# Performance work log

Hardware: AMD Instinct MI355X
Metric: run time of the kernel (lower is better)

## Reference

```python
import jax, jax.numpy as jnp
import numpy as np

N_STREAMS = 8
SINKHORN_ITER = 20
KERNEL_SIZE = 5
BANDWIDTH = 0.5
PAD = KERNEL_SIZE // 2
EPS = 1e-8


def _gaussian_kernel():
    x = jnp.arange(KERNEL_SIZE, dtype=jnp.float32) - KERNEL_SIZE // 2
    xx, yy = jnp.meshgrid(x, x, indexing='ij')
    k = jnp.exp(-(xx ** 2 + yy ** 2) / (2.0 * BANDWIDTH ** 2))
    k = k / k.sum()
    return k.reshape(1, 1, KERNEL_SIZE, KERNEL_SIZE)  # OIHW


def setup_inputs() -> dict:
    key = jax.random.key(0)
    B, H, W = 32, 128, 128
    log_H_res = jax.random.normal(key, (B, N_STREAMS * N_STREAMS, H, W), dtype=jnp.float32)
    return {"log_H_res": log_H_res, "gaussian_kernel": _gaussian_kernel()}


def reference(log_H_res, gaussian_kernel):
    B, C, H, W = log_H_res.shape
    n = N_STREAMS
    H_lin = jnp.exp(log_H_res.reshape(B, n, n, H, W))

    def smooth(m):
        # m: (B, n, H, W) linear-domain marginal; circular pad + 5x5 Gaussian conv
        x = m.reshape(B * n, 1, H, W)
        x = jnp.pad(x, ((0, 0), (0, 0), (PAD, PAD), (PAD, PAD)), mode='wrap')
        y = jax.lax.conv_general_dilated(
            x, gaussian_kernel, window_strides=(1, 1), padding='VALID',
            dimension_numbers=('NCHW', 'OIHW', 'NCHW'))
        return y.reshape(B, n, H, W)

    def body(_, Hl):
        row = smooth(Hl.sum(axis=2))[:, :, None]   # (B, n, 1, H, W)
        Hl = Hl / (row + EPS)
        col = smooth(Hl.sum(axis=1))[:, None]      # (B, 1, n, H, W)
        Hl = Hl / (col + EPS)
        return Hl

    H_lin = jax.lax.fori_loop(0, SINKHORN_ITER, body, H_lin)
    # faithful to original: log then exp with eps stabilization
    H_star = jnp.exp(jnp.log(H_lin + EPS))
    return H_star  # (B, n, n, H, W)
```

## Files before the change

### kernel.cpp

```cpp
#include <hip/hip_runtime.h>

#define NS    8
#define HGT   128
#define WID   128
#define HW    (HGT * WID)
#define BATCH 32
#define EPSV  1e-8f
#define ITERS 20

#define TH   8
#define LH   (TH + 4)
#define LW   132

typedef float4 f4;
typedef _Float16 half4 __attribute__((ext_vector_type(4)));

__global__ __launch_bounds__(256) void k_init(const float* __restrict__ logH,
                                              _Float16* __restrict__ H0h,
                                              float* __restrict__ u,
                                              float* __restrict__ v,
                                              float* __restrict__ mrow) {
    int gid = blockIdx.x * 256 + threadIdx.x;
    int e = gid * 4;
    int p = e & (HW - 1);
    int c = (e >> 14) & 7;
    int b = e >> 17;
    int base = ((b * NS + c) * NS) * HW + p;
    f4 s = {0.f, 0.f, 0.f, 0.f};
#pragma unroll
    for (int j = 0; j < NS; ++j) {
        f4 l = *(const f4*)(logH + base + j * HW);
        f4 ev;
        ev.x = __expf(l.x); ev.y = __expf(l.y);
        ev.z = __expf(l.z); ev.w = __expf(l.w);
        half4 h;
        h.x = (_Float16)ev.x; h.y = (_Float16)ev.y;
        h.z = (_Float16)ev.z; h.w = (_Float16)ev.w;
        *(half4*)(H0h + base + j * HW) = h;
        s.x += ev.x; s.y += ev.y; s.z += ev.z; s.w += ev.w;
    }
    f4 one = {1.f, 1.f, 1.f, 1.f};
    *(f4*)(u + e) = one;
    *(f4*)(v + e) = one;
    *(f4*)(mrow + e) = s;
}

__device__ __forceinline__ void stage_and_smooth(
        const float* __restrict__ m_in, const float* __restrict__ gk,
        float* __restrict__ a, int b, int ty0, int tid,
        float tile[NS][LH][LW], float wk[25], f4 av[NS], bool write_a) {
    if (tid < 25) wk[tid] = gk[tid];

#pragma unroll
    for (int c = 0; c < NS; ++c) {
        const float* src = m_in + (b * NS + c) * HW;
        for (int t = tid; t < LH * 32; t += 256) {
            int ly = t >> 5, lxq = t & 31;
            int gh = (ty0 + ly - 2 + HGT) & (HGT - 1);
            f4 val = *(const f4*)(src + gh * WID + lxq * 4);
            float* dst = &tile[c][ly][2 + lxq * 4];
            dst[0] = val.x; dst[1] = val.y; dst[2] = val.z; dst[3] = val.w;
        }
        if (tid < LH * 4) {
            int ly = tid >> 2, e = tid & 3;
            int gh = (ty0 + ly - 2 + HGT) & (HGT - 1);
            int x  = (e < 2) ? (126 + e) : (e - 2);
            int hx = (e < 2) ? e : (128 + e);
            tile[c][ly][hx] = src[gh * WID + x];
        }
    }
    __syncthreads();

    int lxq = tid & 31;
    int ly  = tid >> 5;
    int p   = (ty0 + ly) * WID + lxq * 4;

#pragma unroll
    for (int c = 0; c < NS; ++c) {
        float s0 = 0.f, s1 = 0.f, s2 = 0.f, s3 = 0.f;
#pragma unroll
        for (int dy = 0; dy < 5; ++dy) {
            const float* row = &tile[c][ly + dy][lxq * 4];
            f4 A = *(const f4*)row;
            f4 B = *(const f4*)(row + 4);
            float vv[8] = {A.x, A.y, A.z, A.w, B.x, B.y, B.z, B.w};
#pragma unroll
            for (int dx = 0; dx < 5; ++dx) {
                float w = wk[dy * 5 + dx];
                s0 += w * vv[dx];
                s1 += w * vv[dx + 1];
                s2 += w * vv[dx + 2];
                s3 += w * vv[dx + 3];
            }
        }
        int ai = (b * NS + c) * HW + p;
        f4 ao = *(const f4*)(a + ai);
        f4 un;
        un.x = ao.x / (s0 + EPSV);
        un.y = ao.y / (s1 + EPSV);
        un.z = ao.z / (s2 + EPSV);
        un.w = ao.w / (s3 + EPSV);
        if (write_a) *(f4*)(a + ai) = un;
        av[c] = un;
    }
}

template <int ROWSTEP>
__global__ __launch_bounds__(256) void k_step(const float* __restrict__ m_in,
                                              float* __restrict__ a,
                                              const float* __restrict__ bvec,
                                              float* __restrict__ m_out,
                                              const _Float16* __restrict__ H0h,
                                              const float* __restrict__ gk) {
    __shared__ float tile[NS][LH][LW];
    __shared__ float wk[25];
    int tid = threadIdx.x;
    int b   = blockIdx.z;
    int ty0 = blockIdx.y * TH;

    f4 av[NS];
    stage_and_smooth(m_in, gk, a, b, ty0, tid, tile, wk, av, true);

    int lxq = tid & 31;
    int ly  = tid >> 5;
    int p   = (ty0 + ly) * WID + lxq * 4;

    f4 acc[NS];
#pragma unroll
    for (int cp = 0; cp < NS; ++cp) acc[cp] = f4{0.f, 0.f, 0.f, 0.f};
    const _Float16* Hb = H0h + b * NS * NS * HW + p;
#pragma unroll
    for (int c = 0; c < NS; ++c) {
        f4 x = av[c];
#pragma unroll
        for (int cp = 0; cp < NS; ++cp) {
            int ch = ROWSTEP ? (c * NS + cp) : (cp * NS + c);
            half4 h = *(const half4*)(Hb + ch * HW);
            acc[cp].x += (float)h.x * x.x;
            acc[cp].y += (float)h.y * x.y;
            acc[cp].z += (float)h.z * x.z;
            acc[cp].w += (float)h.w * x.w;
        }
    }
#pragma unroll
    for (int cp = 0; cp < NS; ++cp) {
        int oi = (b * NS + cp) * HW + p;
        f4 bv = *(const f4*)(bvec + oi);
        f4 o;
        o.x = bv.x * acc[cp].x;
        o.y = bv.y * acc[cp].y;
        o.z = bv.z * acc[cp].z;
        o.w = bv.w * acc[cp].w;
        *(f4*)(m_out + oi) = o;
    }
}

__global__ __launch_bounds__(256) void k_last(const float* __restrict__ m_in,
                                              float* __restrict__ v,
                                              const float* __restrict__ u,
                                              const float* __restrict__ logH,
                                              float* __restrict__ out,
                                              const float* __restrict__ gk) {
    __shared__ float tile[NS][LH][LW];
    __shared__ float wk[25];
    int tid = threadIdx.x;
    int b   = blockIdx.z;
    int ty0 = blockIdx.y * TH;

    f4 av[NS];
    stage_and_smooth(m_in, gk, v, b, ty0, tid, tile, wk, av, false);

    int lxq = tid & 31;
    int ly  = tid >> 5;
    int p   = (ty0 + ly) * WID + lxq * 4;

    const float* Lb = logH + b * NS * NS * HW + p;
    float* Ob = out + b * NS * NS * HW + p;
#pragma unroll
    for (int i = 0; i < NS; ++i) {
        f4 uu = *(const f4*)(u + (b * NS + i) * HW + p);
#pragma unroll
        for (int j = 0; j < NS; ++j) {
            f4 l = *(const f4*)(Lb + (i * NS + j) * HW);
            f4 o;
            o.x = expf(l.x) * uu.x * av[j].x + EPSV;
            o.y = expf(l.y) * uu.y * av[j].y + EPSV;
            o.z = expf(l.z) * uu.z * av[j].z + EPSV;
            o.w = expf(l.w) * uu.w * av[j].w + EPSV;
            *(f4*)(Ob + (i * NS + j) * HW) = o;
        }
    }
}

extern "C" void kernel_launch(void* const* d_in, const int* in_sizes, int n_in,
                              void* d_out, int out_size, void* d_ws, size_t ws_size,
                              hipStream_t stream) {
    const float* logH = (const float*)d_in[0];
    const float* gk   = (const float*)d_in[1];
    float* out = (float*)d_out;
    _Float16* H0h = (_Float16*)d_out;
    float* ws = (float*)d_ws;
    const int VEC = BATCH * NS * HW;
    float* u    = ws;
    float* v    = ws + VEC;
    float* mrow = ws + 2 * VEC;
    float* mcol = ws + 3 * VEC;

    k_init<<<VEC / 4 / 256, 256, 0, stream>>>(logH, H0h, u, v, mrow);

    dim3 grid(1, HGT / TH, BATCH);
    for (int it = 0; it < ITERS; ++it) {
        k_step<1><<<grid, 256, 0, stream>>>(mrow, u, v, mcol, H0h, gk);
        if (it != ITERS - 1) {
            k_step<0><<<grid, 256, 0, stream>>>(mcol, v, u, mrow, H0h, gk);
        } else {
            k_last<<<grid, 256, 0, stream>>>(mcol, v, u, logH, out, gk);
        }
    }
}
```

Before: 1.465 ms.

## Fuse all Sinkhorn iterations into one persistent cooperative kernel with grid sync

Replaces the 41 separate kernel launches with a single cooperative kernel that keeps the u and v scaling vectors in registers across iterations. Stages are separated by grid-wide syncs, which removes launch overhead and the global-memory round trips for u and v. The grid is 16x32 = 512 blocks with 256 threads and about 50KB of shared memory each, so it relies on every block being co-resident. If the cooperative launch fails, the code falls back to the multi-kernel path.

```diff
diff --git a/kernel.cpp b/kernel.cpp
--- a/kernel.cpp
+++ b/kernel.cpp
@@ -1,4 +1,7 @@
 #include <hip/hip_runtime.h>
+#include <hip/hip_cooperative_groups.h>
+
+namespace cg = cooperative_groups;
 
 #define NS    8
 #define HGT   128
@@ -14,6 +17,186 @@
 
 typedef float4 f4;
 typedef _Float16 half4 __attribute__((ext_vector_type(4)));
+
+__device__ __forceinline__ void stage_tile(const float* __restrict__ m_in,
+                                           int b, int ty0, int tid,
+                                           float tile[NS][LH][LW]) {
+#pragma unroll
+    for (int c = 0; c < NS; ++c) {
+        const float* src = m_in + (b * NS + c) * HW;
+        for (int t = tid; t < LH * 32; t += 256) {
+            int ly = t >> 5, lxq = t & 31;
+            int gh = (ty0 + ly - 2 + HGT) & (HGT - 1);
+            f4 val = *(const f4*)(src + gh * WID + lxq * 4);
+            float* dst = &tile[c][ly][2 + lxq * 4];
+            dst[0] = val.x; dst[1] = val.y; dst[2] = val.z; dst[3] = val.w;
+        }
+        if (tid < LH * 4) {
+            int ly = tid >> 2, e = tid & 3;
+            int gh = (ty0 + ly - 2 + HGT) & (HGT - 1);
+            int x  = (e < 2) ? (126 + e) : (e - 2);
+            int hx = (e < 2) ? e : (128 + e);
+            tile[c][ly][hx] = src[gh * WID + x];
+        }
+    }
+}
+
+__device__ __forceinline__ f4 conv5(const float (*tc)[LW], const float* wk,
+                                    int ly, int lxq) {
+    float s0 = 0.f, s1 = 0.f, s2 = 0.f, s3 = 0.f;
+#pragma unroll
+    for (int dy = 0; dy < 5; ++dy) {
+        const float* row = &tc[ly + dy][lxq * 4];
+        f4 A = *(const f4*)row;
+        f4 B = *(const f4*)(row + 4);
+        float vv[8] = {A.x, A.y, A.z, A.w, B.x, B.y, B.z, B.w};
+#pragma unroll
+        for (int dx = 0; dx < 5; ++dx) {
+            float w = wk[dy * 5 + dx];
+            s0 += w * vv[dx];
+            s1 += w * vv[dx + 1];
+            s2 += w * vv[dx + 2];
+            s3 += w * vv[dx + 3];
+        }
+    }
+    return f4{s0, s1, s2, s3};
+}
+
+__global__ __launch_bounds__(256, 2) void k_sink_all(
+        const float* __restrict__ logH, _Float16* __restrict__ H0h,
+        float* __restrict__ mrow, float* __restrict__ mcol,
+        const float* __restrict__ gk, float* __restrict__ out) {
+    cg::grid_group grid = cg::this_grid();
+    __shared__ float tile[NS][LH][LW];
+    __shared__ float wk[25];
+    int tid = threadIdx.x;
+    int ty0 = blockIdx.x * TH;
+    int b   = blockIdx.y;
+    if (tid < 25) wk[tid] = gk[tid];
+
+    int lxq = tid & 31;
+    int ly  = tid >> 5;
+    int p   = (ty0 + ly) * WID + lxq * 4;
+
+    const float* Lb = logH + (b * NS * NS) * HW + p;
+    _Float16*    Hb = H0h  + (b * NS * NS) * HW + p;
+
+    f4 u[NS], v[NS];
+
+#pragma unroll
+    for (int i = 0; i < NS; ++i) {
+        f4 si = {0.f, 0.f, 0.f, 0.f};
+#pragma unroll
+        for (int j = 0; j < NS; ++j) {
+            f4 l = *(const f4*)(Lb + (i * NS + j) * HW);
+            f4 ev;
+            ev.x = __expf(l.x); ev.y = __expf(l.y);
+            ev.z = __expf(l.z); ev.w = __expf(l.w);
+            half4 h;
+            h.x = (_Float16)ev.x; h.y = (_Float16)ev.y;
+            h.z = (_Float16)ev.z; h.w = (_Float16)ev.w;
+            *(half4*)(Hb + (i * NS + j) * HW) = h;
+            si.x += ev.x; si.y += ev.y; si.z += ev.z; si.w += ev.w;
+        }
+        *(f4*)(mrow + (b * NS + i) * HW + p) = si;
+        u[i] = f4{1.f, 1.f, 1.f, 1.f};
+        v[i] = f4{1.f, 1.f, 1.f, 1.f};
+    }
+    grid.sync();
+
+    for (int it = 0; it < ITERS; ++it) {
+        stage_tile(mrow, b, ty0, tid, tile);
+        __syncthreads();
+#pragma unroll
+        for (int c = 0; c < NS; ++c) {
+            f4 s = conv5(tile[c], wk, ly, lxq);
+            u[c].x /= (s.x + EPSV);
+            u[c].y /= (s.y + EPSV);
+            u[c].z /= (s.z + EPSV);
+            u[c].w /= (s.w + EPSV);
+        }
+        {
+            f4 acc[NS];
+#pragma unroll
+            for (int cp = 0; cp < NS; ++cp) acc[cp] = f4{0.f, 0.f, 0.f, 0.f};
+#pragma unroll
+            for (int c = 0; c < NS; ++c) {
+                f4 x = u[c];
+#pragma unroll
+                for (int cp = 0; cp < NS; ++cp) {
+                    half4 h = *(const half4*)(Hb + (c * NS + cp) * HW);
+                    acc[cp].x += (float)h.x * x.x;
+                    acc[cp].y += (float)h.y * x.y;
+                    acc[cp].z += (float)h.z * x.z;
+                    acc[cp].w += (float)h.w * x.w;
+                }
+            }
+#pragma unroll
+            for (int cp = 0; cp < NS; ++cp) {
+                f4 o;
+                o.x = v[cp].x * acc[cp].x;
+                o.y = v[cp].y * acc[cp].y;
+                o.z = v[cp].z * acc[cp].z;
+                o.w = v[cp].w * acc[cp].w;
+                *(f4*)(mcol + (b * NS + cp) * HW + p) = o;
+            }
+        }
+        grid.sync();
+
+        stage_tile(mcol, b, ty0, tid, tile);
+        __syncthreads();
+#pragma unroll
+        for (int c = 0; c < NS; ++c) {
+            f4 s = conv5(tile[c], wk, ly, lxq);
+            v[c].x /= (s.x + EPSV);
+            v[c].y /= (s.y + EPSV);
+            v[c].z /= (s.z + EPSV);
+            v[c].w /= (s.w + EPSV);
+        }
+        if (it != ITERS - 1) {
+            f4 acc[NS];
+#pragma unroll
+            for (int cp = 0; cp < NS; ++cp) acc[cp] = f4{0.f, 0.f, 0.f, 0.f};
+#pragma unroll
+            for (int c = 0; c < NS; ++c) {
+                f4 x = v[c];
+#pragma unroll
+                for (int cp = 0; cp < NS; ++cp) {
+                    half4 h = *(const half4*)(Hb + (cp * NS + c) * HW);
+                    acc[cp].x += (float)h.x * x.x;
+                    acc[cp].y += (float)h.y * x.y;
+                    acc[cp].z += (float)h.z * x.z;
+                    acc[cp].w += (float)h.w * x.w;
+                }
+            }
+#pragma unroll
+            for (int cp = 0; cp < NS; ++cp) {
+                f4 o;
+                o.x = u[cp].x * acc[cp].x;
+                o.y = u[cp].y * acc[cp].y;
+                o.z = u[cp].z * acc[cp].z;
+                o.w = u[cp].w * acc[cp].w;
+                *(f4*)(mrow + (b * NS + cp) * HW + p) = o;
+            }
+            grid.sync();
+        }
+    }
+
+    float* Ob = out + (b * NS * NS) * HW + p;
+#pragma unroll
+    for (int i = 0; i < NS; ++i) {
+#pragma unroll
+        for (int j = 0; j < NS; ++j) {
+            f4 l = *(const f4*)(Lb + (i * NS + j) * HW);
+            f4 o;
+            o.x = expf(l.x) * u[i].x * v[j].x + EPSV;
+            o.y = expf(l.y) * u[i].y * v[j].y + EPSV;
+            o.z = expf(l.z) * u[i].z * v[j].z + EPSV;
+            o.w = expf(l.w) * u[i].w * v[j].w + EPSV;
+            *(f4*)(Ob + (i * NS + j) * HW) = o;
+        }
+    }
+}
 
 __global__ __launch_bounds__(256) void k_init(const float* __restrict__ logH,
                                               _Float16* __restrict__ H0h,
@@ -50,25 +233,7 @@
         float* __restrict__ a, int b, int ty0, int tid,
         float tile[NS][LH][LW], float wk[25], f4 av[NS], bool write_a) {
     if (tid < 25) wk[tid] = gk[tid];
-
-#pragma unroll
-    for (int c = 0; c < NS; ++c) {
-        const float* src = m_in + (b * NS + c) * HW;
-        for (int t = tid; t < LH * 32; t += 256) {
-            int ly = t >> 5, lxq = t & 31;
-            int gh = (ty0 + ly - 2 + HGT) & (HGT - 1);
-            f4 val = *(const f4*)(src + gh * WID + lxq * 4);
-            float* dst = &tile[c][ly][2 + lxq * 4];
-            dst[0] = val.x; dst[1] = val.y; dst[2] = val.z; dst[3] = val.w;
-        }
-        if (tid < LH * 4) {
-            int ly = tid >> 2, e = tid & 3;
-            int gh = (ty0 + ly - 2 + HGT) & (HGT - 1);
-            int x  = (e < 2) ? (126 + e) : (e - 2);
-            int hx = (e < 2) ? e : (128 + e);
-            tile[c][ly][hx] = src[gh * WID + x];
-        }
-    }
+    stage_tile(m_in, b, ty0, tid, tile);
     __syncthreads();
 
     int lxq = tid & 31;
@@ -77,29 +242,14 @@
 
 #pragma unroll
     for (int c = 0; c < NS; ++c) {
-        float s0 = 0.f, s1 = 0.f, s2 = 0.f, s3 = 0.f;
-#pragma unroll
-        for (int dy = 0; dy < 5; ++dy) {
-            const float* row = &tile[c][ly + dy][lxq * 4];
-            f4 A = *(const f4*)row;
-            f4 B = *(const f4*)(row + 4);
-            float vv[8] = {A.x, A.y, A.z, A.w, B.x, B.y, B.z, B.w};
-#pragma unroll
-            for (int dx = 0; dx < 5; ++dx) {
-                float w = wk[dy * 5 + dx];
-                s0 += w * vv[dx];
-                s1 += w * vv[dx + 1];
-                s2 += w * vv[dx + 2];
-                s3 += w * vv[dx + 3];
-            }
-        }
+        f4 s = conv5(tile[c], wk, ly, lxq);
         int ai = (b * NS + c) * HW + p;
         f4 ao = *(const f4*)(a + ai);
         f4 un;
-        un.x = ao.x / (s0 + EPSV);
-        un.y = ao.y / (s1 + EPSV);
-        un.z = ao.z / (s2 + EPSV);
-        un.w = ao.w / (s3 + EPSV);
+        un.x = ao.x / (s.x + EPSV);
+        un.y = ao.y / (s.y + EPSV);
+        un.z = ao.z / (s.z + EPSV);
+        un.w = ao.w / (s.w + EPSV);
         if (write_a) *(f4*)(a + ai) = un;
         av[c] = un;
     }
@@ -201,20 +351,31 @@
     _Float16* H0h = (_Float16*)d_out;
     float* ws = (float*)d_ws;
     const int VEC = BATCH * NS * HW;
-    float* u    = ws;
-    float* v    = ws + VEC;
-    float* mrow = ws + 2 * VEC;
-    float* mcol = ws + 3 * VEC;
-
-    k_init<<<VEC / 4 / 256, 256, 0, stream>>>(logH, H0h, u, v, mrow);
+
+    float* mrow = ws;
+    float* mcol = ws + VEC;
+    void* args[] = {(void*)&logH, (void*)&H0h, (void*)&mrow, (void*)&mcol,
+                    (void*)&gk, (void*)&out};
+    hipError_t err = hipLaunchCooperativeKernel(k_sink_all,
+                                                dim3(HGT / TH, BATCH, 1),
+                                                dim3(256, 1, 1),
+                                                args, 0, stream);
+    if (err == hipSuccess) return;
+
+    float* u     = ws;
+    float* v     = ws + VEC;
+    float* mrow2 = ws + 2 * (size_t)VEC;
+    float* mcol2 = ws + 3 * (size_t)VEC;
+
+    k_init<<<VEC / 4 / 256, 256, 0, stream>>>(logH, H0h, u, v, mrow2);
 
     dim3 grid(1, HGT / TH, BATCH);
     for (int it = 0; it < ITERS; ++it) {
-        k_step<1><<<grid, 256, 0, stream>>>(mrow, u, v, mcol, H0h, gk);
+        k_step<1><<<grid, 256, 0, stream>>>(mrow2, u, v, mcol2, H0h, gk);
         if (it != ITERS - 1) {
-            k_step<0><<<grid, 256, 0, stream>>>(mcol, v, u, mrow, H0h, gk);
+            k_step<0><<<grid, 256, 0, stream>>>(mcol2, v, u, mrow2, H0h, gk);
         } else {
-            k_last<<<grid, 256, 0, stream>>>(mcol, v, u, logH, out, gk);
-        }
-    }
-}
+            k_last<<<grid, 256, 0, stream>>>(mcol2, v, u, logH, out, gk);
+        }
+    }
+}
```

Result: slower. 4.318 ms (+194.8%).

## Use 512-thread blocks with two pixels per thread and specialize the first iteration

Applied to the files above, without the earlier changes.

Blocks grow from 256 to 512 threads, each handling two pixels instead of four, which cuts per-thread register pressure and raises the number of resident waves. The halo loads move to otherwise idle threads so staging no longer loops. The first row and column steps get FIRST specializations that skip reading u and v, and the init kernel no longer fills them with ones. In exchange, each global access is narrower (float2 and half2 instead of float4 and half4), which may lower memory efficiency.

```diff
diff --git a/kernel.cpp b/kernel.cpp
--- a/kernel.cpp
+++ b/kernel.cpp
@@ -13,12 +13,12 @@
 #define LW   132
 
 typedef float4 f4;
+typedef float2 f2;
 typedef _Float16 half4 __attribute__((ext_vector_type(4)));
+typedef _Float16 half2v __attribute__((ext_vector_type(2)));
 
 __global__ __launch_bounds__(256) void k_init(const float* __restrict__ logH,
                                               _Float16* __restrict__ H0h,
-                                              float* __restrict__ u,
-                                              float* __restrict__ v,
                                               float* __restrict__ mrow) {
     int gid = blockIdx.x * 256 + threadIdx.x;
     int e = gid * 4;
@@ -39,155 +39,162 @@
         *(half4*)(H0h + base + j * HW) = h;
         s.x += ev.x; s.y += ev.y; s.z += ev.z; s.w += ev.w;
     }
-    f4 one = {1.f, 1.f, 1.f, 1.f};
-    *(f4*)(u + e) = one;
-    *(f4*)(v + e) = one;
     *(f4*)(mrow + e) = s;
 }
 
-__device__ __forceinline__ void stage_and_smooth(
-        const float* __restrict__ m_in, const float* __restrict__ gk,
-        float* __restrict__ a, int b, int ty0, int tid,
-        float tile[NS][LH][LW], float wk[25], f4 av[NS], bool write_a) {
-    if (tid < 25) wk[tid] = gk[tid];
-
+__device__ __forceinline__ void stage_tile(const float* __restrict__ m_in,
+                                           int b, int ty0, int tid,
+                                           float tile[NS][LH][LW]) {
 #pragma unroll
     for (int c = 0; c < NS; ++c) {
         const float* src = m_in + (b * NS + c) * HW;
-        for (int t = tid; t < LH * 32; t += 256) {
-            int ly = t >> 5, lxq = t & 31;
+        if (tid < LH * 32) {
+            int ly = tid >> 5, lxq = tid & 31;
             int gh = (ty0 + ly - 2 + HGT) & (HGT - 1);
             f4 val = *(const f4*)(src + gh * WID + lxq * 4);
             float* dst = &tile[c][ly][2 + lxq * 4];
             dst[0] = val.x; dst[1] = val.y; dst[2] = val.z; dst[3] = val.w;
-        }
-        if (tid < LH * 4) {
-            int ly = tid >> 2, e = tid & 3;
+        } else if (tid >= 512 - LH * 4) {
+            int t = tid - (512 - LH * 4);
+            int ly = t >> 2, e = t & 3;
             int gh = (ty0 + ly - 2 + HGT) & (HGT - 1);
             int x  = (e < 2) ? (126 + e) : (e - 2);
             int hx = (e < 2) ? e : (128 + e);
             tile[c][ly][hx] = src[gh * WID + x];
         }
     }
-    __syncthreads();
-
-    int lxq = tid & 31;
-    int ly  = tid >> 5;
-    int p   = (ty0 + ly) * WID + lxq * 4;
-
-#pragma unroll
-    for (int c = 0; c < NS; ++c) {
-        float s0 = 0.f, s1 = 0.f, s2 = 0.f, s3 = 0.f;
-#pragma unroll
-        for (int dy = 0; dy < 5; ++dy) {
-            const float* row = &tile[c][ly + dy][lxq * 4];
-            f4 A = *(const f4*)row;
-            f4 B = *(const f4*)(row + 4);
-            float vv[8] = {A.x, A.y, A.z, A.w, B.x, B.y, B.z, B.w};
-#pragma unroll
-            for (int dx = 0; dx < 5; ++dx) {
-                float w = wk[dy * 5 + dx];
-                s0 += w * vv[dx];
-                s1 += w * vv[dx + 1];
-                s2 += w * vv[dx + 2];
-                s3 += w * vv[dx + 3];
-            }
-        }
-        int ai = (b * NS + c) * HW + p;
-        f4 ao = *(const f4*)(a + ai);
-        f4 un;
-        un.x = ao.x / (s0 + EPSV);
-        un.y = ao.y / (s1 + EPSV);
-        un.z = ao.z / (s2 + EPSV);
-        un.w = ao.w / (s3 + EPSV);
-        if (write_a) *(f4*)(a + ai) = un;
-        av[c] = un;
-    }
-}
-
-template <int ROWSTEP>
-__global__ __launch_bounds__(256) void k_step(const float* __restrict__ m_in,
-                                              float* __restrict__ a,
-                                              const float* __restrict__ bvec,
-                                              float* __restrict__ m_out,
-                                              const _Float16* __restrict__ H0h,
-                                              const float* __restrict__ gk) {
+}
+
+__device__ __forceinline__ f2 conv5(const float (*tc)[LW], const float* wk,
+                                    int ly, int lx2) {
+    float s0 = 0.f, s1 = 0.f;
+#pragma unroll
+    for (int dy = 0; dy < 5; ++dy) {
+        const float* row = &tc[ly + dy][lx2 * 2];
+        f2 A = *(const f2*)row;
+        f2 B = *(const f2*)(row + 2);
+        f2 C = *(const f2*)(row + 4);
+        float vv[6] = {A.x, A.y, B.x, B.y, C.x, C.y};
+#pragma unroll
+        for (int dx = 0; dx < 5; ++dx) {
+            float w = wk[dy * 5 + dx];
+            s0 += w * vv[dx];
+            s1 += w * vv[dx + 1];
+        }
+    }
+    return f2{s0, s1};
+}
+
+template <int ROWSTEP, int FIRST>
+__global__ __launch_bounds__(512, 4) void k_step(const float* __restrict__ m_in,
+                                                 float* __restrict__ a,
+                                                 const float* __restrict__ bvec,
+                                                 float* __restrict__ m_out,
+                                                 const _Float16* __restrict__ H0h,
+                                                 const float* __restrict__ gk) {
     __shared__ float tile[NS][LH][LW];
     __shared__ float wk[25];
     int tid = threadIdx.x;
     int b   = blockIdx.z;
     int ty0 = blockIdx.y * TH;
-
-    f4 av[NS];
-    stage_and_smooth(m_in, gk, a, b, ty0, tid, tile, wk, av, true);
-
-    int lxq = tid & 31;
-    int ly  = tid >> 5;
-    int p   = (ty0 + ly) * WID + lxq * 4;
-
-    f4 acc[NS];
-#pragma unroll
-    for (int cp = 0; cp < NS; ++cp) acc[cp] = f4{0.f, 0.f, 0.f, 0.f};
+    if (tid < 25) wk[tid] = gk[tid];
+
+    stage_tile(m_in, b, ty0, tid, tile);
+    __syncthreads();
+
+    int lx2 = tid & 63;
+    int ly  = tid >> 6;
+    int p   = (ty0 + ly) * WID + lx2 * 2;
+
+    f2 av[NS];
+#pragma unroll
+    for (int c = 0; c < NS; ++c) {
+        f2 s = conv5(tile[c], wk, ly, lx2);
+        int ai = (b * NS + c) * HW + p;
+        f2 un;
+        if (FIRST) {
+            un.x = 1.f / (s.x + EPSV);
+            un.y = 1.f / (s.y + EPSV);
+        } else {
+            f2 ao = *(const f2*)(a + ai);
+            un.x = ao.x / (s.x + EPSV);
+            un.y = ao.y / (s.y + EPSV);
+        }
+        *(f2*)(a + ai) = un;
+        av[c] = un;
+    }
+
+    f2 acc[NS];
+#pragma unroll
+    for (int cp = 0; cp < NS; ++cp) acc[cp] = f2{0.f, 0.f};
     const _Float16* Hb = H0h + b * NS * NS * HW + p;
 #pragma unroll
     for (int c = 0; c < NS; ++c) {
-        f4 x = av[c];
+        f2 x = av[c];
 #pragma unroll
         for (int cp = 0; cp < NS; ++cp) {
             int ch = ROWSTEP ? (c * NS + cp) : (cp * NS + c);
-            half4 h = *(const half4*)(Hb + ch * HW);
+            half2v h = *(const half2v*)(Hb + ch * HW);
             acc[cp].x += (float)h.x * x.x;
             acc[cp].y += (float)h.y * x.y;
-            acc[cp].z += (float)h.z * x.z;
-            acc[cp].w += (float)h.w * x.w;
         }
     }
 #pragma unroll
     for (int cp = 0; cp < NS; ++cp) {
         int oi = (b * NS + cp) * HW + p;
-        f4 bv = *(const f4*)(bvec + oi);
-        f4 o;
-        o.x = bv.x * acc[cp].x;
-        o.y = bv.y * acc[cp].y;
-        o.z = bv.z * acc[cp].z;
-        o.w = bv.w * acc[cp].w;
-        *(f4*)(m_out + oi) = o;
-    }
-}
-
-__global__ __launch_bounds__(256) void k_last(const float* __restrict__ m_in,
-                                              float* __restrict__ v,
-                                              const float* __restrict__ u,
-                                              const float* __restrict__ logH,
-                                              float* __restrict__ out,
-                                              const float* __restrict__ gk) {
+        f2 o;
+        if (ROWSTEP && FIRST) {
+            o = acc[cp];
+        } else {
+            f2 bv = *(const f2*)(bvec + oi);
+            o.x = bv.x * acc[cp].x;
+            o.y = bv.y * acc[cp].y;
+        }
+        *(f2*)(m_out + oi) = o;
+    }
+}
+
+__global__ __launch_bounds__(512, 4) void k_last(const float* __restrict__ m_in,
+                                                 const float* __restrict__ v,
+                                                 const float* __restrict__ u,
+                                                 const float* __restrict__ logH,
+                                                 float* __restrict__ out,
+                                                 const float* __restrict__ gk) {
     __shared__ float tile[NS][LH][LW];
     __shared__ float wk[25];
     int tid = threadIdx.x;
     int b   = blockIdx.z;
     int ty0 = blockIdx.y * TH;
-
-    f4 av[NS];
-    stage_and_smooth(m_in, gk, v, b, ty0, tid, tile, wk, av, false);
-
-    int lxq = tid & 31;
-    int ly  = tid >> 5;
-    int p   = (ty0 + ly) * WID + lxq * 4;
+    if (tid < 25) wk[tid] = gk[tid];
+
+    stage_tile(m_in, b, ty0, tid, tile);
+    __syncthreads();
+
+    int lx2 = tid & 63;
+    int ly  = tid >> 6;
+    int p   = (ty0 + ly) * WID + lx2 * 2;
+
+    f2 av[NS];
+#pragma unroll
+    for (int c = 0; c < NS; ++c) {
+        f2 s = conv5(tile[c], wk, ly, lx2);
+        f2 vo = *(const f2*)(v + (b * NS + c) * HW + p);
+        av[c].x = vo.x / (s.x + EPSV);
+        av[c].y = vo.y / (s.y + EPSV);
+    }
 
     const float* Lb = logH + b * NS * NS * HW + p;
     float* Ob = out + b * NS * NS * HW + p;
 #pragma unroll
     for (int i = 0; i < NS; ++i) {
-        f4 uu = *(const f4*)(u + (b * NS + i) * HW + p);
+        f2 uu = *(const f2*)(u + (b * NS + i) * HW + p);
 #pragma unroll
         for (int j = 0; j < NS; ++j) {
-            f4 l = *(const f4*)(Lb + (i * NS + j) * HW);
-            f4 o;
+            f2 l = *(const f2*)(Lb + (i * NS + j) * HW);
+            f2 o;
             o.x = expf(l.x) * uu.x * av[j].x + EPSV;
             o.y = expf(l.y) * uu.y * av[j].y + EPSV;
-            o.z = expf(l.z) * uu.z * av[j].z + EPSV;
-            o.w = expf(l.w) * uu.w * av[j].w + EPSV;
-            *(f4*)(Ob + (i * NS + j) * HW) = o;
+            *(f2*)(Ob + (i * NS + j) * HW) = o;
         }
     }
 }
@@ -203,18 +210,20 @@
     const int VEC = BATCH * NS * HW;
     float* u    = ws;
     float* v    = ws + VEC;
-    float* mrow = ws + 2 * VEC;
-    float* mcol = ws + 3 * VEC;
-
-    k_init<<<VEC / 4 / 256, 256, 0, stream>>>(logH, H0h, u, v, mrow);
+    float* mrow = ws + 2 * (size_t)VEC;
+    float* mcol = ws + 3 * (size_t)VEC;
+
+    k_init<<<VEC / 4 / 256, 256, 0, stream>>>(logH, H0h, mrow);
 
     dim3 grid(1, HGT / TH, BATCH);
-    for (int it = 0; it < ITERS; ++it) {
-        k_step<1><<<grid, 256, 0, stream>>>(mrow, u, v, mcol, H0h, gk);
+    k_step<1, 1><<<grid, 512, 0, stream>>>(mrow, u, v, mcol, H0h, gk);
+    k_step<0, 1><<<grid, 512, 0, stream>>>(mcol, v, u, mrow, H0h, gk);
+    for (int it = 1; it < ITERS; ++it) {
+        k_step<1, 0><<<grid, 512, 0, stream>>>(mrow, u, v, mcol, H0h, gk);
         if (it != ITERS - 1) {
-            k_step<0><<<grid, 256, 0, stream>>>(mcol, v, u, mrow, H0h, gk);
+            k_step<0, 0><<<grid, 512, 0, stream>>>(mcol, v, u, mrow, H0h, gk);
         } else {
-            k_last<<<grid, 256, 0, stream>>>(mcol, v, u, logH, out, gk);
-        }
-    }
-}
+            k_last<<<grid, 512, 0, stream>>>(mcol, v, u, logH, out, gk);
+        }
+    }
+}
```

Result: faster. 1.361 ms (-7.1%).
